# Kernel tuning notes

Hardware: AMD Instinct MI355X
Metric: run time of the kernel (lower is better)

Reference implementation:

```python
import jax, jax.numpy as jnp
import numpy as np

NUM_GRAPHS = 100  # batch of graphs for pooling (dgl.max_nodes / WeightAndSum)


def _glorot(k, shape):
    lim = np.sqrt(6.0 / (shape[0] + shape[1])).astype(np.float32)
    return jax.random.uniform(k, shape, jnp.float32, -lim, lim)


def setup_inputs() -> dict:
    key = jax.random.key(0)
    ks = jax.random.split(key, 10)
    N, E, D, H = 100000, 1600000, 128, 128
    node_feats = jax.random.normal(ks[0], (N, D), dtype=jnp.float32)
    src = jax.random.randint(ks[1], (E,), 0, N, dtype=jnp.int32)
    dst = jax.random.randint(ks[2], (E,), 0, N, dtype=jnp.int32)
    graph_ids = jnp.sort(jax.random.randint(ks[3], (N,), 0, NUM_GRAPHS, dtype=jnp.int32))
    W1 = _glorot(ks[4], (D, H)); b1 = jnp.zeros((H,), jnp.float32)
    W2 = _glorot(ks[5], (H, H)); b2 = jnp.zeros((H,), jnp.float32)
    W3 = _glorot(ks[6], (H, H)); b3 = jnp.zeros((H,), jnp.float32)
    W_pool = _glorot(ks[7], (H, 1)); b_pool = jnp.zeros((1,), jnp.float32)
    return {"node_feats": node_feats, "src": src, "dst": dst, "graph_ids": graph_ids,
            "W1": W1, "b1": b1, "W2": W2, "b2": b2, "W3": W3, "b3": b3,
            "W_pool": W_pool, "b_pool": b_pool}


def _gcn_layer(h, W, b, src, dst, norm_src, norm_dst, N):
    # DGL GraphConv, norm='both': D_dst^{-1/2} (A^T (D_src^{-1/2} X W)) + b
    h = (h * norm_src[:, None]) @ W                      # [N, H]
    agg = jax.ops.segment_sum(h[src], dst, num_segments=N)  # gather + scatter-add
    return agg * norm_dst[:, None] + b


def reference(node_feats, src, dst, graph_ids, W1, b1, W2, b2, W3, b3, W_pool, b_pool):
    N = node_feats.shape[0]
    # dgl.add_self_loop (allow_zero_in_degree=False)
    loops = jnp.arange(N, dtype=src.dtype)
    src_sl = jnp.concatenate([src, loops])
    dst_sl = jnp.concatenate([dst, loops])
    ones = jnp.ones(src_sl.shape, jnp.float32)
    out_deg = jax.ops.segment_sum(ones, src_sl, num_segments=N)
    in_deg = jax.ops.segment_sum(ones, dst_sl, num_segments=N)
    norm_src = jax.lax.rsqrt(jnp.maximum(out_deg, 1.0))
    norm_dst = jax.lax.rsqrt(jnp.maximum(in_deg, 1.0))
    h = node_feats
    for W, b in ((W1, b1), (W2, b2), (W3, b3)):
        h = jax.nn.relu(_gcn_layer(h, W, b, src_sl, dst_sl, norm_src, norm_dst, N))
    # pooling_func: WeightAndSum (sigmoid-gated weighted sum per graph) + max_nodes
    w = jax.nn.sigmoid(h @ W_pool + b_pool)              # [N, 1]
    g_sum = jax.ops.segment_sum(h * w, graph_ids, num_segments=NUM_GRAPHS)
    g_max = jax.ops.segment_max(h, graph_ids, num_segments=NUM_GRAPHS)
    return jnp.concatenate([g_sum, g_max], axis=1)       # [G, 2H]
```

## Files before the change

kernel.cpp:

```cpp
#include <hip/hip_runtime.h>
#include <hip/hip_bf16.h>

#define DIM 128
#define CAP 64
#define NBMAX 64
#define BCAP 36864
#define CSPLIT 8

typedef __attribute__((ext_vector_type(8))) short bf16x8;
typedef __attribute__((ext_vector_type(4))) float f32x4;
typedef __bf16 bf16x2 __attribute__((ext_vector_type(2)));
union U16 { uint4 u; bf16x8 b; };
union UB { unsigned u; bf16x2 h; };

__device__ __forceinline__ unsigned short f2bf(float f) {
    unsigned u = __float_as_uint(f);
    unsigned r = (u + 0x7fffu + ((u >> 16) & 1u)) >> 16;
    return (unsigned short)r;
}
__device__ __forceinline__ unsigned pack2bf(float a, float b) {
    return (unsigned)f2bf(a) | ((unsigned)f2bf(b) << 16);
}
__device__ __forceinline__ float2 unpack2bf(unsigned v) {
    float2 r;
    r.x = __uint_as_float(v << 16);
    r.y = __uint_as_float(v & 0xffff0000u);
    return r;
}
__device__ __forceinline__ void accum8s(float* acc, uint4 v, float s) {
    float2 f0 = unpack2bf(v.x), f1 = unpack2bf(v.y);
    float2 f2 = unpack2bf(v.z), f3 = unpack2bf(v.w);
    acc[0] += s * f0.x; acc[1] += s * f0.y; acc[2] += s * f1.x; acc[3] += s * f1.y;
    acc[4] += s * f2.x; acc[5] += s * f2.y; acc[6] += s * f3.x; acc[7] += s * f3.y;
}
__device__ __forceinline__ void accum8m(float* acc, uint4 v, float s) {
    UB w0, w1, w2, w3;
    w0.u = v.x; w1.u = v.y; w2.u = v.z; w3.u = v.w;
    acc[0] = fmaf((float)w0.h[0], s, acc[0]);
    acc[1] = fmaf((float)w0.h[1], s, acc[1]);
    acc[2] = fmaf((float)w1.h[0], s, acc[2]);
    acc[3] = fmaf((float)w1.h[1], s, acc[3]);
    acc[4] = fmaf((float)w2.h[0], s, acc[4]);
    acc[5] = fmaf((float)w2.h[1], s, acc[5]);
    acc[6] = fmaf((float)w3.h[0], s, acc[6]);
    acc[7] = fmaf((float)w3.h[1], s, acc[7]);
}

__global__ __launch_bounds__(256) void k_bin(const int* __restrict__ src,
                                             const int* __restrict__ dst, int E,
                                             unsigned* __restrict__ binD,
                                             unsigned short* __restrict__ binS,
                                             int* __restrict__ cntD,
                                             int* __restrict__ cntS, int NB, int binGrid,
                                             const float* __restrict__ W1,
                                             const float* __restrict__ W2,
                                             const float* __restrict__ W3,
                                             unsigned* __restrict__ wT1g,
                                             unsigned* __restrict__ wT2g,
                                             unsigned* __restrict__ wT3g) {
    __shared__ int hD[NBMAX], hS[NBMAX], bD[NBMAX], bS[NBMAX];
    int t = threadIdx.x;
    if ((int)blockIdx.x >= binGrid) {
        int w = blockIdx.x - binGrid;
        const float* Wsrc = (w == 0) ? W1 : (w == 1) ? W2 : W3;
        unsigned* wTg = (w == 0) ? wT1g : (w == 1) ? wT2g : wT3g;
        int n = t >> 1;
        int kp0 = (t & 1) * 32;
#pragma unroll
        for (int i = 0; i < 32; i++) {
            int kp = kp0 + i;
            wTg[n * 64 + kp] = pack2bf(Wsrc[(2 * kp) * DIM + n], Wsrc[(2 * kp + 1) * DIM + n]);
        }
        return;
    }
    if (t < NB) { hD[t] = 0; hS[t] = 0; }
    __syncthreads();
    int e0 = blockIdx.x * 1024 + t * 4;
    int s[4], d[4];
    bool v[4];
#pragma unroll
    for (int i = 0; i < 4; i++) {
        v[i] = (e0 + i) < E;
        s[i] = 0; d[i] = 0;
        if (v[i]) { s[i] = src[e0 + i]; d[i] = dst[e0 + i]; }
    }
#pragma unroll
    for (int i = 0; i < 4; i++) {
        if (v[i]) {
            atomicAdd(&hD[d[i] >> 11], 1);
            atomicAdd(&hS[s[i] >> 11], 1);
        }
    }
    __syncthreads();
    if (t < NB) {
        bD[t] = atomicAdd(&cntD[t], hD[t]);
        bS[t] = atomicAdd(&cntS[t], hS[t]);
        hD[t] = 0; hS[t] = 0;
    }
    __syncthreads();
#pragma unroll
    for (int i = 0; i < 4; i++) {
        if (v[i]) {
            int bd = d[i] >> 11;
            int r = atomicAdd(&hD[bd], 1);
            int idx = bD[bd] + r;
            if (idx < BCAP)
                binD[bd * BCAP + idx] = ((unsigned)(d[i] & 2047) << 17) | (unsigned)s[i];
            int bs = s[i] >> 11;
            int r2 = atomicAdd(&hS[bs], 1);
            int idx2 = bS[bs] + r2;
            if (idx2 < BCAP) binS[bs * BCAP + idx2] = (unsigned short)(s[i] & 2047);
        }
    }
}

__global__ __launch_bounds__(256) void k_mega(const unsigned* __restrict__ binD,
                                              const unsigned short* __restrict__ binS,
                                              const int* __restrict__ cntD,
                                              const int* __restrict__ cntS,
                                              int* __restrict__ in_cnt,
                                              int* __restrict__ out_cnt,
                                              int* __restrict__ csr_pad,
                                              const float* __restrict__ x,
                                              const unsigned* __restrict__ wT1g,
                                              unsigned* __restrict__ xwb, int N,
                                              int NB) {
    __shared__ __align__(16) char smem[34816];
    int bid = blockIdx.x;
    int t = threadIdx.x;

    if (bid < NB * CSPLIT) {
        int b = bid / CSPLIT;
        int sub = bid - b * CSPLIT;
        int* h = (int*)smem;
        int* bArr = ((int*)smem) + 2048;
        for (int j = t; j < 2048; j += 256) h[j] = 0;
        __syncthreads();
        int base = b << 11;
        int nE = cntD[b];
        if (nE > BCAP) nE = BCAP;
        int chunk = (nE + CSPLIT - 1) / CSPLIT;
        int i0 = sub * chunk;
        int i1 = i0 + chunk;
        if (i1 > nE) i1 = nE;
        const unsigned* bb = &binD[b * BCAP];
        for (int i = i0 + t * 4; i < i1; i += 1024) {
            unsigned e[4];
            int k = i1 - i;
            if (k > 4) k = 4;
#pragma unroll
            for (int j = 0; j < 4; j++)
                if (j < k) e[j] = bb[i + j];
#pragma unroll
            for (int j = 0; j < 4; j++)
                if (j < k) atomicAdd(&h[e[j] >> 17], 1);
        }
        __syncthreads();
        for (int j = t; j < 2048; j += 256) {
            int hv = h[j];
            bArr[j] = hv ? atomicAdd(&in_cnt[base + j], hv) : 0;
            h[j] = 0;
        }
        __syncthreads();
        for (int i = i0 + t * 4; i < i1; i += 1024) {
            unsigned e[4];
            int k = i1 - i;
            if (k > 4) k = 4;
#pragma unroll
            for (int j = 0; j < 4; j++)
                if (j < k) e[j] = bb[i + j];
#pragma unroll
            for (int j = 0; j < 4; j++)
                if (j < k) {
                    int dl = (int)(e[j] >> 17);
                    int pos = bArr[dl] + atomicAdd(&h[dl], 1);
                    if (pos < CAP)
                        csr_pad[(size_t)(base + dl) * CAP + pos] = (int)(e[j] & 0x1FFFFu);
                }
        }
        return;
    }
    if (bid < 2 * NB * CSPLIT) {
        int bb2 = bid - NB * CSPLIT;
        int b = bb2 / CSPLIT;
        int sub = bb2 - b * CSPLIT;
        int* hist = (int*)smem;
        for (int j = t; j < 2048; j += 256) hist[j] = 0;
        __syncthreads();
        int base = b << 11;
        int nE = cntS[b];
        if (nE > BCAP) nE = BCAP;
        int chunk = (nE + CSPLIT - 1) / CSPLIT;
        int i0 = sub * chunk;
        int i1 = i0 + chunk;
        if (i1 > nE) i1 = nE;
        const unsigned short* bs = &binS[b * BCAP];
        for (int i = i0 + t * 4; i < i1; i += 1024) {
            unsigned short e[4];
            int k = i1 - i;
            if (k > 4) k = 4;
#pragma unroll
            for (int j = 0; j < 4; j++)
                if (j < k) e[j] = bs[i + j];
#pragma unroll
            for (int j = 0; j < 4; j++)
                if (j < k) atomicAdd(&hist[(int)e[j]], 1);
        }
        __syncthreads();
        for (int j = t; j < 2048; j += 256) {
            int hv = hist[j];
            if (hv) atomicAdd(&out_cnt[base + j], hv);
        }
        return;
    }
    int gb = bid - 2 * NB * CSPLIT;
    unsigned* wT = (unsigned*)smem;
#pragma unroll
    for (int i = 0; i < 8; i++) {
        int idx = t + i * 256;
        int row = idx >> 4;
        int col = idx & 15;
        *(uint4*)&wT[row * 68 + col * 4] = ((const uint4*)wT1g)[idx];
    }
    __syncthreads();
    int wave = t >> 6, lane = t & 63;
    int quad = lane >> 4, c = lane & 15;
    int m = gb * 64 + wave * 16 + c;
    bool mv = m < N;
    f32x4 acc[8];
#pragma unroll
    for (int i = 0; i < 8; i++) acc[i] = (f32x4){0.f, 0.f, 0.f, 0.f};

#pragma unroll
    for (int ks = 0; ks < 4; ks++) {
        U16 av;
        if (mv) {
            const float4* xr = (const float4*)&x[(size_t)m * DIM + ks * 32 + quad * 8];
            float4 f0 = xr[0], f1 = xr[1];
            av.u.x = pack2bf(f0.x, f0.y);
            av.u.y = pack2bf(f0.z, f0.w);
            av.u.z = pack2bf(f1.x, f1.y);
            av.u.w = pack2bf(f1.z, f1.w);
        } else {
            av.u = make_uint4(0, 0, 0, 0);
        }
#pragma unroll
        for (int cb = 0; cb < 8; cb++) {
            U16 bv;
            bv.u = *(const uint4*)&wT[(cb * 16 + c) * 68 + ks * 16 + quad * 4];
            acc[cb] = __builtin_amdgcn_mfma_f32_16x16x32_bf16(av.b, bv.b, acc[cb], 0, 0, 0);
        }
    }
    int rowBase = gb * 64 + wave * 16 + quad * 4;
#pragma unroll
    for (int r = 0; r < 4; r++) {
        int rowN = rowBase + r;
#pragma unroll
        for (int cb = 0; cb < 8; cb++) {
            float v = acc[cb][r];
            float vn = __shfl_xor(v, 1, 64);
            if (((c & 1) == 0) && rowN < N)
                xwb[rowN * 64 + cb * 8 + (c >> 1)] = pack2bf(v, vn);
        }
    }
}

__global__ __launch_bounds__(256) void k_nrm(const int* __restrict__ out_cnt,
                                             float* __restrict__ nsv, int N) {
    int i = (blockIdx.x * 256 + threadIdx.x) * 4;
    if (i + 3 < N) {
        int4 d = *(const int4*)&out_cnt[i];
        float4 r;
        r.x = rsqrtf((float)(d.x + 1));
        r.y = rsqrtf((float)(d.y + 1));
        r.z = rsqrtf((float)(d.z + 1));
        r.w = rsqrtf((float)(d.w + 1));
        *(float4*)&nsv[i] = r;
    } else {
        for (int j = i; j < N && j < i + 4; j++) nsv[j] = rsqrtf((float)(out_cnt[j] + 1));
    }
}

template <int MODE>
__device__ __forceinline__ void agg_body(const uint4* __restrict__ xwb4,
                                         const int* __restrict__ in_cnt,
                                         const int* __restrict__ csr_pad,
                                         const float* __restrict__ nsv,
                                         const float* __restrict__ bias,
                                         uint4* __restrict__ hb4,
                                         const float* __restrict__ Wp,
                                         const float* __restrict__ bp,
                                         float* __restrict__ wg, int N) {
    int wid = (blockIdx.x * 256 + threadIdx.x) >> 6;
    int lane = threadIdx.x & 63;
    int g = lane >> 4, c = lane & 15;
    int n = wid * 4 + g;
    bool nv = n < N;
    int deg_true = nv ? in_cnt[n] : 0;
    int deg = deg_true > CAP ? CAP : deg_true;
    float ndv = rsqrtf((float)(deg_true + 1));
    const int* row = csr_pad + (size_t)n * CAP;

    float acc[8];
#pragma unroll
    for (int i = 0; i < 8; i++) acc[i] = 0.f;

    if (nv) {
        float s0 = (MODE == 0) ? nsv[n] : ndv;
        accum8m(acc, xwb4[(size_t)n * 16 + c], s0);
    }
    for (int p = 0; p < deg; p += 16) {
        int4 r0 = *(const int4*)&row[p];
        int4 r1 = *(const int4*)&row[p + 4];
        int4 r2 = *(const int4*)&row[p + 8];
        int4 r3 = *(const int4*)&row[p + 12];
        int sidx[16];
        sidx[0] = r0.x;  sidx[1] = r0.y;  sidx[2] = r0.z;  sidx[3] = r0.w;
        sidx[4] = r1.x;  sidx[5] = r1.y;  sidx[6] = r1.z;  sidx[7] = r1.w;
        sidx[8] = r2.x;  sidx[9] = r2.y;  sidx[10] = r2.z; sidx[11] = r2.w;
        sidx[12] = r3.x; sidx[13] = r3.y; sidx[14] = r3.z; sidx[15] = r3.w;
        uint4 gv[16];
        float sc[16];
#pragma unroll
        for (int u = 0; u < 16; u++) {
            bool pv = (p + u) < deg;
            int s = pv ? sidx[u] : n;
            gv[u] = xwb4[(size_t)s * 16 + c];
            if (MODE == 0)
                sc[u] = pv ? nsv[s] : 0.f;
            else
                sc[u] = pv ? ndv : 0.f;
        }
#pragma unroll
        for (int u = 0; u < 16; u++) accum8m(acc, gv[u], sc[u]);
    }

    float mul = (MODE == 0) ? ndv : 1.f;
    float4 b0 = ((const float4*)bias)[2 * c];
    float4 b1 = ((const float4*)bias)[2 * c + 1];
    float o[8];
    o[0] = fmaxf(acc[0] * mul + b0.x, 0.f);
    o[1] = fmaxf(acc[1] * mul + b0.y, 0.f);
    o[2] = fmaxf(acc[2] * mul + b0.z, 0.f);
    o[3] = fmaxf(acc[3] * mul + b0.w, 0.f);
    o[4] = fmaxf(acc[4] * mul + b1.x, 0.f);
    o[5] = fmaxf(acc[5] * mul + b1.y, 0.f);
    o[6] = fmaxf(acc[6] * mul + b1.z, 0.f);
    o[7] = fmaxf(acc[7] * mul + b1.w, 0.f);
    if (nv) {
        uint4 w;
        w.x = pack2bf(o[0], o[1]);
        w.y = pack2bf(o[2], o[3]);
        w.z = pack2bf(o[4], o[5]);
        w.w = pack2bf(o[6], o[7]);
        hb4[(size_t)n * 16 + c] = w;
    }
    if (MODE == 2) {
        float4 w0 = ((const float4*)Wp)[2 * c];
        float4 w1 = ((const float4*)Wp)[2 * c + 1];
        float s = o[0] * w0.x + o[1] * w0.y + o[2] * w0.z + o[3] * w0.w +
                  o[4] * w1.x + o[5] * w1.y + o[6] * w1.z + o[7] * w1.w;
        s += __shfl_xor(s, 1, 64);
        s += __shfl_xor(s, 2, 64);
        s += __shfl_xor(s, 4, 64);
        s += __shfl_xor(s, 8, 64);
        if (nv && c == 0) wg[n] = 1.f / (1.f + expf(-(s + bp[0])));
    }
}

__global__ __launch_bounds__(256) void k_agg1(const uint4* __restrict__ xwb4,
                                              const int* __restrict__ in_cnt,
                                              const int* __restrict__ csr_pad,
                                              const float* __restrict__ nsv,
                                              const float* __restrict__ bias,
                                              uint4* __restrict__ hb4, int N) {
    agg_body<0>(xwb4, in_cnt, csr_pad, nsv, bias, hb4, nullptr, nullptr, nullptr, N);
}

__global__ __launch_bounds__(256) void k_agg(const uint4* __restrict__ xwb4,
                                             const int* __restrict__ in_cnt,
                                             const int* __restrict__ csr_pad,
                                             const float* __restrict__ bias,
                                             uint4* __restrict__ hb4, int N) {
    agg_body<1>(xwb4, in_cnt, csr_pad, nullptr, bias, hb4, nullptr, nullptr, nullptr, N);
}

__global__ __launch_bounds__(256) void k_agg_gate(const uint4* __restrict__ xwb4,
                                                  const int* __restrict__ in_cnt,
                                                  const int* __restrict__ csr_pad,
                                                  const float* __restrict__ bias,
                                                  uint4* __restrict__ hb4,
                                                  const float* __restrict__ Wp,
                                                  const float* __restrict__ bp,
                                                  float* __restrict__ wg, int N) {
    agg_body<2>(xwb4, in_cnt, csr_pad, nullptr, bias, hb4, Wp, bp, wg, N);
}

__global__ __launch_bounds__(256) void k_xw_mfma(const unsigned* __restrict__ hb,
                                                 const int* __restrict__ out_cnt,
                                                 const unsigned* __restrict__ wTg,
                                                 unsigned* __restrict__ xwb, int N) {
    __shared__ unsigned wT[128 * 68];
    int t = threadIdx.x;
#pragma unroll
    for (int i = 0; i < 8; i++) {
        int idx = t + i * 256;
        int row = idx >> 4;
        int col = idx & 15;
        *(uint4*)&wT[row * 68 + col * 4] = ((const uint4*)wTg)[idx];
    }
    __syncthreads();
    int wave = t >> 6, lane = t & 63;
    int quad = lane >> 4, c = lane & 15;
    int m = blockIdx.x * 64 + wave * 16 + c;
    bool mv = m < N;
    f32x4 acc[8];
#pragma unroll
    for (int i = 0; i < 8; i++) acc[i] = (f32x4){0.f, 0.f, 0.f, 0.f};

#pragma unroll
    for (int ks = 0; ks < 4; ks++) {
        U16 av;
        if (mv) av.u = *(const uint4*)&hb[m * 64 + ks * 16 + quad * 4];
        else av.u = make_uint4(0, 0, 0, 0);
#pragma unroll
        for (int cb = 0; cb < 8; cb++) {
            U16 bv;
            bv.u = *(const uint4*)&wT[(cb * 16 + c) * 68 + ks * 16 + quad * 4];
            acc[cb] = __builtin_amdgcn_mfma_f32_16x16x32_bf16(av.b, bv.b, acc[cb], 0, 0, 0);
        }
    }
    int rowBase = blockIdx.x * 64 + wave * 16 + quad * 4;
#pragma unroll
    for (int r = 0; r < 4; r++) {
        int rowN = rowBase + r;
        float nrm = (rowN < N) ? rsqrtf((float)(out_cnt[rowN] + 1)) : 0.f;
#pragma unroll
        for (int cb = 0; cb < 8; cb++) {
            float v = acc[cb][r] * nrm;
            float vn = __shfl_xor(v, 1, 64);
            if (((c & 1) == 0) && rowN < N)
                xwb[rowN * 64 + cb * 8 + (c >> 1)] = pack2bf(v, vn);
        }
    }
}

__device__ __forceinline__ int lower_bound(const int* a, int n, int key) {
    int lo = 0, hi = n;
    while (lo < hi) {
        int m = (lo + hi) >> 1;
        if (a[m] < key) lo = m + 1;
        else hi = m;
    }
    return lo;
}

__global__ __launch_bounds__(64) void k_pool(const unsigned* __restrict__ hb,
                                             const float* __restrict__ wg,
                                             const int* __restrict__ gids,
                                             float* __restrict__ out, int N) {
    int g = blockIdx.x >> 4;
    int part = blockIdx.x & 15;
    int t = threadIdx.x;
    int start = lower_bound(gids, N, g);
    int end = lower_bound(gids, N, g + 1);
    float2 sum = {0.f, 0.f}, mx = {0.f, 0.f};
    for (int n = start + part; n < end; n += 16) {
        float w = wg[n];
        float2 v = unpack2bf(hb[n * 64 + t]);
        sum.x += v.x * w;
        sum.y += v.y * w;
        mx.x = fmaxf(mx.x, v.x);
        mx.y = fmaxf(mx.y, v.y);
    }
    atomicAdd(&out[g * 256 + 2 * t], sum.x);
    atomicAdd(&out[g * 256 + 2 * t + 1], sum.y);
    atomicMax((int*)&out[g * 256 + 128 + 2 * t], __float_as_int(mx.x));
    atomicMax((int*)&out[g * 256 + 128 + 2 * t + 1], __float_as_int(mx.y));
}

extern "C" void kernel_launch(void* const* d_in, const int* in_sizes, int n_in,
                              void* d_out, int out_size, void* d_ws, size_t ws_size,
                              hipStream_t stream) {
    const float* node_feats = (const float*)d_in[0];
    const int* src = (const int*)d_in[1];
    const int* dst = (const int*)d_in[2];
    const int* gids = (const int*)d_in[3];
    const float* W1 = (const float*)d_in[4];
    const float* b1 = (const float*)d_in[5];
    const float* W2 = (const float*)d_in[6];
    const float* b2 = (const float*)d_in[7];
    const float* W3 = (const float*)d_in[8];
    const float* b3 = (const float*)d_in[9];
    const float* Wp = (const float*)d_in[10];
    const float* bp = (const float*)d_in[11];
    float* out = (float*)d_out;

    const int N = in_sizes[3];
    const int E = in_sizes[1];
    const int G = out_size / 256;
    const int NB = (N + 2047) >> 11;

    char* ws = (char*)d_ws;
    size_t o = 0;
    int* cntD = (int*)(ws + o);          o += NBMAX * 4;
    int* cntS = (int*)(ws + o);          o += NBMAX * 4;
    int* in_cnt = (int*)(ws + o);        o += (size_t)N * 4;
    int* out_cnt = (int*)(ws + o);       o += (size_t)N * 4;
    size_t zero_bytes = o;
    float* wg = (float*)(ws + o);        o += (size_t)N * 4;
    float* nsv = (float*)(ws + o);       o += (size_t)N * 4;
    o = (o + 15) & ~15ull;
    unsigned* wT1g = (unsigned*)(ws + o); o += 8192 * 4;
    unsigned* wT2g = (unsigned*)(ws + o); o += 8192 * 4;
    unsigned* wT3g = (unsigned*)(ws + o); o += 8192 * 4;
    unsigned* binD = (unsigned*)(ws + o); o += (size_t)NBMAX * BCAP * 4;
    unsigned short* binS = (unsigned short*)(ws + o); o += (size_t)NBMAX * BCAP * 2;
    o = (o + 15) & ~15ull;
    int* csr_pad = (int*)(ws + o);       o += (size_t)N * CAP * 4;
    unsigned* xwb = (unsigned*)(ws + o); o += (size_t)N * 64 * 4;
    unsigned* hb = (unsigned*)(ws + o);  o += (size_t)N * 64 * 4;
    (void)ws_size;

    (void)hipMemsetAsync(d_ws, 0, zero_bytes, stream);
    (void)hipMemsetAsync(d_out, 0, (size_t)out_size * 4, stream);

    int binGrid = (E + 1023) / 1024;
    int mmGrid = (N + 63) / 64;
    int aggGrid = (N + 15) / 16;
    int nrmGrid = (N + 1023) / 1024;

    k_bin<<<binGrid + 3, 256, 0, stream>>>(src, dst, E, binD, binS, cntD, cntS, NB, binGrid,
                                           W1, W2, W3, wT1g, wT2g, wT3g);
    k_mega<<<2 * NB * CSPLIT + mmGrid, 256, 0, stream>>>(binD, binS, cntD, cntS, in_cnt,
                                                         out_cnt, csr_pad, node_feats,
                                                         wT1g, xwb, N, NB);
    k_nrm<<<nrmGrid, 256, 0, stream>>>(out_cnt, nsv, N);
    k_agg1<<<aggGrid, 256, 0, stream>>>((const uint4*)xwb, in_cnt, csr_pad, nsv, b1,
                                        (uint4*)hb, N);
    k_xw_mfma<<<mmGrid, 256, 0, stream>>>(hb, out_cnt, wT2g, xwb, N);
    k_agg<<<aggGrid, 256, 0, stream>>>((const uint4*)xwb, in_cnt, csr_pad, b2,
                                       (uint4*)hb, N);
    k_xw_mfma<<<mmGrid, 256, 0, stream>>>(hb, out_cnt, wT3g, xwb, N);
    k_agg_gate<<<aggGrid, 256, 0, stream>>>((const uint4*)xwb, in_cnt, csr_pad, b3,
                                            (uint4*)hb, Wp, bp, wg, N);
    k_pool<<<G * 16, 64, 0, stream>>>(hb, wg, gids, out, N);
}
```

Measured before the change: 444.8 us.

## Fuse next-layer MFMA weight transform into GCN aggregation kernels

Removes the separate k_xw_mfma launches by having each aggregation kernel multiply its freshly aggregated node rows by the next layer's weight matrix via MFMA, using lane shuffles to assemble A operands and an LDS-staged weight tile. This avoids writing and rereading the intermediate hidden features and the extra launches. In exchange each aggregation block now stages a 34KB weight tile in LDS and pays a barrier, lowering occupancy of the latency-bound gather, and the MFMA runs with 12 of 16 rows zero-padded.

```diff
diff --git a/kernel.cpp b/kernel.cpp
--- a/kernel.cpp
+++ b/kernel.cpp
@@ -26,12 +26,6 @@
     r.x = __uint_as_float(v << 16);
     r.y = __uint_as_float(v & 0xffff0000u);
     return r;
-}
-__device__ __forceinline__ void accum8s(float* acc, uint4 v, float s) {
-    float2 f0 = unpack2bf(v.x), f1 = unpack2bf(v.y);
-    float2 f2 = unpack2bf(v.z), f3 = unpack2bf(v.w);
-    acc[0] += s * f0.x; acc[1] += s * f0.y; acc[2] += s * f1.x; acc[3] += s * f1.y;
-    acc[4] += s * f2.x; acc[5] += s * f2.y; acc[6] += s * f3.x; acc[7] += s * f3.y;
 }
 __device__ __forceinline__ void accum8m(float* acc, uint4 v, float s) {
     UB w0, w1, w2, w3;
@@ -282,32 +276,47 @@
 }
 
 template <int MODE>
-__device__ __forceinline__ void agg_body(const uint4* __restrict__ xwb4,
+__device__ __forceinline__ void agg_body(const uint4* __restrict__ src4,
                                          const int* __restrict__ in_cnt,
                                          const int* __restrict__ csr_pad,
                                          const float* __restrict__ nsv,
                                          const float* __restrict__ bias,
-                                         uint4* __restrict__ hb4,
+                                         const unsigned* __restrict__ wTg,
+                                         unsigned* __restrict__ wTlds,
+                                         unsigned* __restrict__ outw,
                                          const float* __restrict__ Wp,
                                          const float* __restrict__ bp,
                                          float* __restrict__ wg, int N) {
-    int wid = (blockIdx.x * 256 + threadIdx.x) >> 6;
-    int lane = threadIdx.x & 63;
+    int t = threadIdx.x;
+    if (MODE != 2) {
+#pragma unroll
+        for (int i = 0; i < 8; i++) {
+            int idx = t + i * 256;
+            int rrow = idx >> 4;
+            int col = idx & 15;
+            *(uint4*)&wTlds[rrow * 68 + col * 4] = ((const uint4*)wTg)[idx];
+        }
+    }
+    int wid = (blockIdx.x * 256 + t) >> 6;
+    int lane = t & 63;
     int g = lane >> 4, c = lane & 15;
-    int n = wid * 4 + g;
-    bool nv = n < N;
+    int n0 = wid * 4 + g;
+    bool nv = n0 < N;
+    int n = nv ? n0 : 0;
     int deg_true = nv ? in_cnt[n] : 0;
     int deg = deg_true > CAP ? CAP : deg_true;
     float ndv = rsqrtf((float)(deg_true + 1));
     const int* row = csr_pad + (size_t)n * CAP;
 
+    if (MODE != 2) __syncthreads();
+
     float acc[8];
 #pragma unroll
     for (int i = 0; i < 8; i++) acc[i] = 0.f;
 
     if (nv) {
         float s0 = (MODE == 0) ? nsv[n] : ndv;
-        accum8m(acc, xwb4[(size_t)n * 16 + c], s0);
+        accum8m(acc, src4[(size_t)n * 16 + c], s0);
     }
     for (int p = 0; p < deg; p += 16) {
         int4 r0 = *(const int4*)&row[p];
@@ -325,7 +334,7 @@
         for (int u = 0; u < 16; u++) {
             bool pv = (p + u) < deg;
             int s = pv ? sidx[u] : n;
-            gv[u] = xwb4[(size_t)s * 16 + c];
+            gv[u] = src4[(size_t)s * 16 + c];
             if (MODE == 0)
                 sc[u] = pv ? nsv[s] : 0.f;
             else
@@ -347,15 +356,14 @@
     o[5] = fmaxf(acc[5] * mul + b1.y, 0.f);
     o[6] = fmaxf(acc[6] * mul + b1.z, 0.f);
     o[7] = fmaxf(acc[7] * mul + b1.w, 0.f);
-    if (nv) {
-        uint4 w;
-        w.x = pack2bf(o[0], o[1]);
-        w.y = pack2bf(o[2], o[3]);
-        w.z = pack2bf(o[4], o[5]);
-        w.w = pack2bf(o[6], o[7]);
-        hb4[(size_t)n * 16 + c] = w;
-    }
+    uint4 w;
+    w.x = pack2bf(o[0], o[1]);
+    w.y = pack2bf(o[2], o[3]);
+    w.z = pack2bf(o[4], o[5]);
+    w.w = pack2bf(o[6], o[7]);
+
     if (MODE == 2) {
+        if (nv) ((uint4*)outw)[(size_t)n * 16 + c] = w;
         float4 w0 = ((const float4*)Wp)[2 * c];
         float4 w1 = ((const float4*)Wp)[2 * c + 1];
         float s = o[0] * w0.x + o[1] * w0.y + o[2] * w0.z + o[3] * w0.w +
@@ -365,6 +373,42 @@
         s += __shfl_xor(s, 4, 64);
         s += __shfl_xor(s, 8, 64);
         if (nv && c == 0) wg[n] = 1.f / (1.f + expf(-(s + bp[0])));
+    } else {
+        float my_nsv = nv ? nsv[n] : 0.f;
+        f32x4 acc2[8];
+#pragma unroll
+        for (int i = 0; i < 8; i++) acc2[i] = (f32x4){0.f, 0.f, 0.f, 0.f};
+        int q = lane >> 4;
+        int r = lane & 15;
+#pragma unroll
+        for (int ks = 0; ks < 4; ks++) {
+            int srcl = (r & 3) * 16 + ks * 4 + q;
+            U16 av;
+            av.u.x = __shfl(w.x, srcl, 64);
+            av.u.y = __shfl(w.y, srcl, 64);
+            av.u.z = __shfl(w.z, srcl, 64);
+            av.u.w = __shfl(w.w, srcl, 64);
+            if (r >= 4) av.u = make_uint4(0, 0, 0, 0);
+#pragma unroll
+            for (int cb = 0; cb < 8; cb++) {
+                U16 bv;
+                bv.u = *(const uint4*)&wTlds[(cb * 16 + r) * 68 + ks * 16 + q * 4];
+                acc2[cb] = __builtin_amdgcn_mfma_f32_16x16x32_bf16(av.b, bv.b, acc2[cb], 0, 0, 0);
+            }
+        }
+        int nodeBase = wid * 4;
+#pragma unroll
+        for (int r2 = 0; r2 < 4; r2++) {
+            int rowN = nodeBase + r2;
+            float nrm = __shfl(my_nsv, r2 << 4, 64);
+#pragma unroll
+            for (int cb = 0; cb < 8; cb++) {
+                float v = acc2[cb][r2] * nrm;
+                float vn = __shfl_xor(v, 1, 64);
+                if ((lane < 16) && ((lane & 1) == 0) && rowN < N)
+                    outw[(size_t)rowN * 64 + cb * 8 + (lane >> 1)] = pack2bf(v, vn);
+            }
+        }
     }
 }
 
@@ -373,76 +417,32 @@
                                               const int* __restrict__ csr_pad,
                                               const float* __restrict__ nsv,
                                               const float* __restrict__ bias,
-                                              uint4* __restrict__ hb4, int N) {
-    agg_body<0>(xwb4, in_cnt, csr_pad, nsv, bias, hb4, nullptr, nullptr, nullptr, N);
-}
-
-__global__ __launch_bounds__(256) void k_agg(const uint4* __restrict__ xwb4,
-                                             const int* __restrict__ in_cnt,
-                                             const int* __restrict__ csr_pad,
-                                             const float* __restrict__ bias,
-                                             uint4* __restrict__ hb4, int N) {
-    agg_body<1>(xwb4, in_cnt, csr_pad, nullptr, bias, hb4, nullptr, nullptr, nullptr, N);
+                                              const unsigned* __restrict__ wT2g,
+                                              unsigned* __restrict__ hb, int N) {
+    __shared__ unsigned wT[128 * 68];
+    agg_body<0>(xwb4, in_cnt, csr_pad, nsv, bias, wT2g, wT, hb, nullptr, nullptr, nullptr, N);
+}
+
+__global__ __launch_bounds__(256) void k_agg2(const uint4* __restrict__ hb4,
+                                              const int* __restrict__ in_cnt,
+                                              const int* __restrict__ csr_pad,
+                                              const float* __restrict__ nsv,
+                                              const float* __restrict__ bias,
+                                              const unsigned* __restrict__ wT3g,
+                                              unsigned* __restrict__ xwb, int N) {
+    __shared__ unsigned wT[128 * 68];
+    agg_body<1>(hb4, in_cnt, csr_pad, nsv, bias, wT3g, wT, xwb, nullptr, nullptr, nullptr, N);
 }
 
 __global__ __launch_bounds__(256) void k_agg_gate(const uint4* __restrict__ xwb4,
                                                   const int* __restrict__ in_cnt,
                                                   const int* __restrict__ csr_pad,
                                                   const float* __restrict__ bias,
-                                                  uint4* __restrict__ hb4,
+                                                  unsigned* __restrict__ hb,
                                                   const float* __restrict__ Wp,
                                                   const float* __restrict__ bp,
                                                   float* __restrict__ wg, int N) {
-    agg_body<2>(xwb4, in_cnt, csr_pad, nullptr, bias, hb4, Wp, bp, wg, N);
-}
-
-__global__ __launch_bounds__(256) void k_xw_mfma(const unsigned* __restrict__ hb,
-                                                 const int* __restrict__ out_cnt,
-                                                 const unsigned* __restrict__ wTg,
-                                                 unsigned* __restrict__ xwb, int N) {
-    __shared__ unsigned wT[128 * 68];
-    int t = threadIdx.x;
-#pragma unroll
-    for (int i = 0; i < 8; i++) {
-        int idx = t + i * 256;
-        int row = idx >> 4;
-        int col = idx & 15;
-        *(uint4*)&wT[row * 68 + col * 4] = ((const uint4*)wTg)[idx];
-    }
-    __syncthreads();
-    int wave = t >> 6, lane = t & 63;
-    int quad = lane >> 4, c = lane & 15;
-    int m = blockIdx.x * 64 + wave * 16 + c;
-    bool mv = m < N;
-    f32x4 acc[8];
-#pragma unroll
-    for (int i = 0; i < 8; i++) acc[i] = (f32x4){0.f, 0.f, 0.f, 0.f};
-
-#pragma unroll
-    for (int ks = 0; ks < 4; ks++) {
-        U16 av;
-        if (mv) av.u = *(const uint4*)&hb[m * 64 + ks * 16 + quad * 4];
-        else av.u = make_uint4(0, 0, 0, 0);
-#pragma unroll
-        for (int cb = 0; cb < 8; cb++) {
-            U16 bv;
-            bv.u = *(const uint4*)&wT[(cb * 16 + c) * 68 + ks * 16 + quad * 4];
-            acc[cb] = __builtin_amdgcn_mfma_f32_16x16x32_bf16(av.b, bv.b, acc[cb], 0, 0, 0);
-        }
-    }
-    int rowBase = blockIdx.x * 64 + wave * 16 + quad * 4;
-#pragma unroll
-    for (int r = 0; r < 4; r++) {
-        int rowN = rowBase + r;
-        float nrm = (rowN < N) ? rsqrtf((float)(out_cnt[rowN] + 1)) : 0.f;
-#pragma unroll
-        for (int cb = 0; cb < 8; cb++) {
-            float v = acc[cb][r] * nrm;
-            float vn = __shfl_xor(v, 1, 64);
-            if (((c & 1) == 0) && rowN < N)
-                xwb[rowN * 64 + cb * 8 + (c >> 1)] = pack2bf(v, vn);
-        }
-    }
+    agg_body<2>(xwb4, in_cnt, csr_pad, nullptr, bias, nullptr, nullptr, hb, Wp, bp, wg, N);
 }
 
 __device__ __forceinline__ int lower_bound(const int* a, int n, int key) {
@@ -537,12 +537,10 @@
                                                          wT1g, xwb, N, NB);
     k_nrm<<<nrmGrid, 256, 0, stream>>>(out_cnt, nsv, N);
     k_agg1<<<aggGrid, 256, 0, stream>>>((const uint4*)xwb, in_cnt, csr_pad, nsv, b1,
-                                        (uint4*)hb, N);
-    k_xw_mfma<<<mmGrid, 256, 0, stream>>>(hb, out_cnt, wT2g, xwb, N);
-    k_agg<<<aggGrid, 256, 0, stream>>>((const uint4*)xwb, in_cnt, csr_pad, b2,
-                                       (uint4*)hb, N);
-    k_xw_mfma<<<mmGrid, 256, 0, stream>>>(hb, out_cnt, wT3g, xwb, N);
+                                        wT2g, hb, N);
+    k_agg2<<<aggGrid, 256, 0, stream>>>((const uint4*)hb, in_cnt, csr_pad, nsv, b2,
+                                        wT3g, xwb, N);
     k_agg_gate<<<aggGrid, 256, 0, stream>>>((const uint4*)xwb, in_cnt, csr_pad, b3,
-                                            (uint4*)hb, Wp, bp, wg, N);
+                                            hb, Wp, bp, wg, N);
     k_pool<<<G * 16, 64, 0, stream>>>(hb, wg, gids, out, N);
 }
```

New measurement: 456.9 us. 1.03x slower.
